# Optimization experiments

Measured on AMD Instinct MI355X. Metric: run time of the kernel, lower is better.

Reference implementation:

```python
import jax, jax.numpy as jnp
import numpy as np
from jax import lax

B, C, H, W = 8, 64, 112, 112
MID = 256
K = 5
DIL = 2
PAD = 4


def setup_inputs() -> dict:
    key = jax.random.key(0)
    k1, k2, k3, k4, k5 = jax.random.split(key, 5)
    x = jax.random.normal(k1, (B, C, H, W), dtype=jnp.float32)
    # conv1: in_channel -> 256, k=5, dilation=2, pad=4
    w1 = jax.random.normal(k2, (MID, C, K, K), dtype=jnp.float32) * (1.0 / np.sqrt(C * K * K))
    b1 = jax.random.normal(k3, (MID,), dtype=jnp.float32) * 0.01
    # conv2: 256 -> 25, 1x1
    w2 = jax.random.normal(k4, (K * K, MID, 1, 1), dtype=jnp.float32) * (1.0 / np.sqrt(MID))
    b2 = jax.random.normal(k5, (K * K,), dtype=jnp.float32) * 0.01
    return {"x": x, "w1": w1, "b1": b1, "w2": w2, "b2": b2}


def reference(x, w1, b1, w2, b2):
    # attention-weight branch
    k = lax.conv_general_dilated(
        x, w1, window_strides=(1, 1), padding=[(PAD, PAD), (PAD, PAD)],
        rhs_dilation=(DIL, DIL), dimension_numbers=("NCHW", "OIHW", "NCHW"))
    k = k + b1[None, :, None, None]                       # [B, 256, H, W]
    k = jnp.einsum("oi,bihw->bohw", w2[:, :, 0, 0], k) + b2[None, :, None, None]
    k = jax.nn.softmax(k, axis=1)                          # [B, 25, H, W]

    # fused local attention: weighted sum over the 5x5 dilated neighborhood.
    # Equivalent to unfold(x, k=5, dilation=2, pad=4) * k summed over the 25 taps,
    # but never materializes the [B, C, 25, H, W] unfolded tensor.
    xp = jnp.pad(x, ((0, 0), (0, 0), (PAD, PAD), (PAD, PAD)))
    out = jnp.zeros_like(x)
    for idx in range(K * K):
        i, j = divmod(idx, K)
        patch = lax.dynamic_slice(xp, (0, 0, DIL * i, DIL * j), (B, C, H, W))
        out = out + patch * k[:, idx:idx + 1]              # broadcast over C
    return out
```

## Files before the change

kernel.cpp:

```cpp
#include <hip/hip_runtime.h>

#define BATCH 8
#define CH    64
#define HH    112
#define WW    112
#define HW    (HH * WW)
#define NP    (BATCH * HW)
#define TAPS  25
#define MIDC  256
#define PIX   64
#define CPW   16
#define NBLK  (NP / PIX)
#define NXCD  8
#define CPX   (NBLK / NXCD)

#define WEFF_N (CH * TAPS * TAPS)
__global__ __launch_bounds__(256) void weff_kernel(
    const float* __restrict__ w1, const float* __restrict__ b1,
    const float* __restrict__ w2, const float* __restrict__ b2,
    float* __restrict__ weff, float* __restrict__ beff) {
  const int id = blockIdx.x * 256 + threadIdx.x;
  if (id < WEFF_N) {
    const int tap = id % TAPS;
    const int t2  = id / TAPS;
    const int o   = t2 % TAPS;
    const int c   = t2 / TAPS;
    const float* w2o = w2 + o * MIDC;
    float a0 = 0.f, a1 = 0.f;
    #pragma unroll 4
    for (int mid = 0; mid < MIDC; mid += 2) {
      a0 = fmaf(w1[(mid * CH + c) * TAPS + tap],       w2o[mid],     a0);
      a1 = fmaf(w1[((mid + 1) * CH + c) * TAPS + tap], w2o[mid + 1], a1);
    }
    weff[(c * TAPS + tap) * TAPS + o] = a0 + a1;
  } else if (id < WEFF_N + TAPS) {
    const int o = id - WEFF_N;
    const float* w2o = w2 + o * MIDC;
    float b = b2[o];
    for (int mid = 0; mid < MIDC; ++mid) b = fmaf(w2o[mid], b1[mid], b);
    beff[o] = b;
  }
}

__global__ __launch_bounds__(256, 6) void picanet_main(
    const float* __restrict__ x, const float* __restrict__ weff,
    const float* __restrict__ beff, float* __restrict__ out) {
  __shared__ float red[4 * PIX * TAPS];

  const int lane = threadIdx.x & 63;
  const int wave = threadIdx.x >> 6;
  const int c0 = __builtin_amdgcn_readfirstlane(wave * CPW);

  const int lb = (blockIdx.x & (NXCD - 1)) * CPX + (blockIdx.x >> 3);
  const int p  = lb * PIX + lane;
  const int b  = p / HW;
  const int hw = p % HW;
  const int h  = hw / WW;
  const int w  = hw % WW;

  const float* xb = x + (size_t)b * CH * HW + (size_t)c0 * HW;
  const float* wc = weff + (size_t)c0 * TAPS * TAPS;

  float s[TAPS];
  #pragma unroll
  for (int o = 0; o < TAPS; ++o) s[o] = 0.f;

  #pragma unroll 1
  for (int tap = 0; tap < TAPS; ++tap) {
    int i = tap / 5, j = tap % 5;
    int yy = h + 2 * i - 4;
    int xx = w + 2 * j - 4;
    if (yy >= 0 && yy < HH && xx >= 0 && xx < WW) {
      int offt = yy * WW + xx;
      const float* wt = wc + tap * TAPS;
      #pragma unroll
      for (int c = 0; c < CPW; ++c) {
        float xv = xb[(size_t)c * HW + offt];
        const float* wp = wt + c * (TAPS * TAPS);
        #pragma unroll
        for (int o = 0; o < TAPS; ++o) s[o] = fmaf(xv, wp[o], s[o]);
      }
    }
  }

  #pragma unroll
  for (int o = 0; o < TAPS; ++o) red[(wave * PIX + lane) * TAPS + o] = s[o];
  __syncthreads();

  if (lane < CPW) {
    const int px = (wave << 4) + lane;
    float t[TAPS];
    #pragma unroll
    for (int o = 0; o < TAPS; ++o)
      t[o] = red[px * TAPS + o] + red[(PIX + px) * TAPS + o] +
             red[(2 * PIX + px) * TAPS + o] + red[(3 * PIX + px) * TAPS + o] +
             beff[o];
    float m = t[0];
    #pragma unroll
    for (int o = 1; o < TAPS; ++o) m = fmaxf(m, t[o]);
    float sum = 0.f;
    #pragma unroll
    for (int o = 0; o < TAPS; ++o) { t[o] = __expf(t[o] - m); sum += t[o]; }
    float inv = 1.f / sum;
    #pragma unroll
    for (int o = 0; o < TAPS; ++o) red[px * TAPS + o] = t[o] * inv;
  }
  __syncthreads();

  float acc[CPW];
  #pragma unroll
  for (int c = 0; c < CPW; ++c) acc[c] = 0.f;

  #pragma unroll 1
  for (int tap = 0; tap < TAPS; ++tap) {
    int i = tap / 5, j = tap % 5;
    int yy = h + 2 * i - 4;
    int xx = w + 2 * j - 4;
    float sv = red[lane * TAPS + tap];
    if (yy >= 0 && yy < HH && xx >= 0 && xx < WW) {
      int offt = yy * WW + xx;
      #pragma unroll
      for (int c = 0; c < CPW; ++c)
        acc[c] = fmaf(sv, xb[(size_t)c * HW + offt], acc[c]);
    }
  }

  float* ob = out + (size_t)b * CH * HW + (size_t)c0 * HW + hw;
  #pragma unroll
  for (int c = 0; c < CPW; ++c) ob[c * HW] = acc[c];
}

extern "C" void kernel_launch(void* const* d_in, const int* in_sizes, int n_in,
                              void* d_out, int out_size, void* d_ws, size_t ws_size,
                              hipStream_t stream) {
  const float* x  = (const float*)d_in[0];
  const float* w1 = (const float*)d_in[1];
  const float* b1 = (const float*)d_in[2];
  const float* w2 = (const float*)d_in[3];
  const float* b2 = (const float*)d_in[4];
  float* out  = (float*)d_out;
  float* weff = (float*)d_ws;
  float* beff = weff + CH * TAPS * TAPS;

  weff_kernel<<<(WEFF_N + TAPS + 255) / 256, 256, 0, stream>>>(w1, b1, w2, b2, weff, beff);
  picanet_main<<<NBLK, 256, 0, stream>>>(x, weff, beff, out);
}
```

Measured before the change: 234.0 us.

## Software-pipeline x loads across taps, branchless masking, redundant per-wave softmax

The logit accumulation loop now double-buffers x loads in two half-channel groups, prefetching the next tap's values while FMAs run on the current ones. Out-of-bounds taps are handled by clamped addresses and zero masks instead of branches. Every wave now computes the softmax redundantly for all 64 pixels, which removes the second __syncthreads and the lane<16 serial section. The weighted-sum loop is fully unrolled and reads softmax weights from registers. The costs are higher register pressure, possible occupancy loss at launch bounds of 6, and four times the softmax arithmetic.

New measurement: 368.8 us. +57.6%, slower.

```diff
diff --git a/kernel.cpp b/kernel.cpp
--- a/kernel.cpp
+++ b/kernel.cpp
@@ -10,6 +10,7 @@
 #define MIDC  256
 #define PIX   64
 #define CPW   16
+#define HCPW  8
 #define NBLK  (NP / PIX)
 #define NXCD  8
 #define CPX   (NBLK / NXCD)
@@ -59,70 +60,100 @@
   const int w  = hw % WW;
 
   const float* xb = x + (size_t)b * CH * HW + (size_t)c0 * HW;
-  const float* wc = weff + (size_t)c0 * TAPS * TAPS;
+  const float* wc = weff + (size_t)c0 * (TAPS * TAPS);
 
   float s[TAPS];
   #pragma unroll
   for (int o = 0; o < TAPS; ++o) s[o] = 0.f;
 
+  float xA[HCPW], xB[HCPW];
+  int  offc, offn;
+  bool okc, okn;
+
+  {
+    int yy = h - 4, xx = w - 4;
+    okc  = (yy >= 0) & (xx >= 0);
+    offc = okc ? (yy * WW + xx) : hw;
+  }
+  #pragma unroll
+  for (int c = 0; c < HCPW; ++c) xA[c] = xb[(size_t)c * HW + offc];
+
   #pragma unroll 1
-  for (int tap = 0; tap < TAPS; ++tap) {
-    int i = tap / 5, j = tap % 5;
-    int yy = h + 2 * i - 4;
-    int xx = w + 2 * j - 4;
-    if (yy >= 0 && yy < HH && xx >= 0 && xx < WW) {
-      int offt = yy * WW + xx;
-      const float* wt = wc + tap * TAPS;
+  for (int t = 0; t < TAPS; ++t) {
+    #pragma unroll
+    for (int c = 0; c < HCPW; ++c) xB[c] = xb[(size_t)(c + HCPW) * HW + offc];
+
+    #pragma unroll
+    for (int c = 0; c < HCPW; ++c) {
+      float xm = okc ? xA[c] : 0.f;
+      const float* wp = wc + ((size_t)c * TAPS + t) * TAPS;
       #pragma unroll
-      for (int c = 0; c < CPW; ++c) {
-        float xv = xb[(size_t)c * HW + offt];
-        const float* wp = wt + c * (TAPS * TAPS);
-        #pragma unroll
-        for (int o = 0; o < TAPS; ++o) s[o] = fmaf(xv, wp[o], s[o]);
-      }
+      for (int o = 0; o < TAPS; ++o) s[o] = fmaf(xm, wp[o], s[o]);
     }
+
+    {
+      int tn = (t < TAPS - 1) ? t + 1 : TAPS - 1;
+      int i = tn / 5, j = tn % 5;
+      int yy = h + 2 * i - 4;
+      int xx = w + 2 * j - 4;
+      okn  = (yy >= 0) & (yy < HH) & (xx >= 0) & (xx < WW);
+      offn = okn ? (yy * WW + xx) : hw;
+    }
+    #pragma unroll
+    for (int c = 0; c < HCPW; ++c) xA[c] = xb[(size_t)c * HW + offn];
+
+    #pragma unroll
+    for (int c = 0; c < HCPW; ++c) {
+      float xm = okc ? xB[c] : 0.f;
+      const float* wp = wc + ((size_t)(c + HCPW) * TAPS + t) * TAPS;
+      #pragma unroll
+      for (int o = 0; o < TAPS; ++o) s[o] = fmaf(xm, wp[o], s[o]);
+    }
+
+    offc = offn; okc = okn;
   }
 
   #pragma unroll
   for (int o = 0; o < TAPS; ++o) red[(wave * PIX + lane) * TAPS + o] = s[o];
   __syncthreads();
 
-  if (lane < CPW) {
-    const int px = (wave << 4) + lane;
-    float t[TAPS];
-    #pragma unroll
-    for (int o = 0; o < TAPS; ++o)
-      t[o] = red[px * TAPS + o] + red[(PIX + px) * TAPS + o] +
-             red[(2 * PIX + px) * TAPS + o] + red[(3 * PIX + px) * TAPS + o] +
-             beff[o];
-    float m = t[0];
-    #pragma unroll
-    for (int o = 1; o < TAPS; ++o) m = fmaxf(m, t[o]);
-    float sum = 0.f;
-    #pragma unroll
-    for (int o = 0; o < TAPS; ++o) { t[o] = __expf(t[o] - m); sum += t[o]; }
-    float inv = 1.f / sum;
-    #pragma unroll
-    for (int o = 0; o < TAPS; ++o) red[px * TAPS + o] = t[o] * inv;
+  float m = -1e30f;
+  #pragma unroll
+  for (int o = 0; o < TAPS; ++o) {
+    float v = red[lane * TAPS + o] + red[(PIX + lane) * TAPS + o] +
+              red[(2 * PIX + lane) * TAPS + o] +
+              red[(3 * PIX + lane) * TAPS + o] + beff[o];
+    s[o] = v;
+    m = fmaxf(m, v);
   }
-  __syncthreads();
+  float sum = 0.f;
+  #pragma unroll
+  for (int o = 0; o < TAPS; ++o) { s[o] = __expf(s[o] - m); sum += s[o]; }
+  float inv = 1.f / sum;
+  #pragma unroll
+  for (int o = 0; o < TAPS; ++o) {
+    int i = o / 5, j = o % 5;
+    int yy = h + 2 * i - 4;
+    int xx = w + 2 * j - 4;
+    bool ok = (yy >= 0) & (yy < HH) & (xx >= 0) & (xx < WW);
+    s[o] = ok ? s[o] * inv : 0.f;
+  }
 
   float acc[CPW];
   #pragma unroll
   for (int c = 0; c < CPW; ++c) acc[c] = 0.f;
 
-  #pragma unroll 1
-  for (int tap = 0; tap < TAPS; ++tap) {
-    int i = tap / 5, j = tap % 5;
+  #pragma unroll
+  for (int t = 0; t < TAPS; ++t) {
+    int i = t / 5, j = t % 5;
     int yy = h + 2 * i - 4;
     int xx = w + 2 * j - 4;
-    float sv = red[lane * TAPS + tap];
-    if (yy >= 0 && yy < HH && xx >= 0 && xx < WW) {
-      int offt = yy * WW + xx;
-      #pragma unroll
-      for (int c = 0; c < CPW; ++c)
-        acc[c] = fmaf(sv, xb[(size_t)c * HW + offt], acc[c]);
-    }
+    bool ok = (yy >= 0) & (yy < HH) & (xx >= 0) & (xx < WW);
+    int offt = ok ? yy * WW + xx : hw;
+    float sv = s[t];
+    #pragma unroll
+    for (int c = 0; c < CPW; ++c)
+      acc[c] = fmaf(sv, xb[(size_t)c * HW + offt], acc[c]);
   }
 
   float* ob = out + (size_t)b * CH * HW + (size_t)c0 * HW + hw;
```
